# Optimization experiments

Measured on AMD Instinct MI355X. Metric: run time of the kernel, lower is better.

## Reference

```python
import jax, jax.numpy as jnp
import numpy as np

N, E, IN_DIM, OUT_DIM, T = 100000, 1600000, 128, 64, 8
V_THRESHOLD = 1.0
EPS = 1e-7

# ---- Lorentz manifold (curvature -1), time coordinate first ----

def _linner(a, b):
    # Lorentzian inner product <a,b>_L = -a0*b0 + sum_i ai*bi
    return -a[..., 0] * b[..., 0] + jnp.sum(a[..., 1:] * b[..., 1:], axis=-1)

def _proju(z, u):
    # project ambient vector u to tangent space at z (<z,z>_L = -1)
    return u + _linner(z, u)[..., None] * z

def _expmap(z, u):
    un = jnp.sqrt(jnp.maximum(_linner(u, u), EPS))[..., None]
    return jnp.cosh(un) * z + jnp.sinh(un) * u / un

def _dist0(z):
    # geodesic distance to origin o=(1,0,...,0): arccosh(-<o,z>_L) = arccosh(z0)
    return jnp.arccosh(jnp.maximum(z[..., 0], 1.0 + EPS))

# ---- GCNConv (torch_geometric semantics: self-loops + symmetric norm) ----

def _gcn(x, edge_index, W, b):
    src, dst = edge_index[0], edge_index[1]
    loops = jnp.arange(N, dtype=src.dtype)
    src = jnp.concatenate([src, loops])
    dst = jnp.concatenate([dst, loops])
    deg = jax.ops.segment_sum(jnp.ones_like(dst, dtype=x.dtype), dst, num_segments=N)
    dinv = jax.lax.rsqrt(jnp.maximum(deg, 1.0))  # deg >= 1 due to self-loops
    norm = dinv[src] * dinv[dst]                 # [E+N]
    h = x @ W                                    # [N, OUT_DIM]
    out = jax.ops.segment_sum(norm[:, None] * h[src], dst, num_segments=N)
    return out + b


def setup_inputs() -> dict:
    key = jax.random.key(0)
    k1, k2, k3 = jax.random.split(key, 3)
    x = jax.random.normal(k1, (N, IN_DIM), dtype=jnp.float32)
    edge_index = jax.random.randint(k2, (2, E), 0, N, dtype=jnp.int32)
    W = jax.random.normal(k3, (IN_DIM, OUT_DIM), dtype=jnp.float32) / np.sqrt(IN_DIM)
    b = jnp.zeros((OUT_DIM,), dtype=jnp.float32)
    return {"x": x, "edge_index": edge_index, "W": W, "b": b}


def reference(x, edge_index, W, b):
    h = _gcn(x, edge_index, W, b)                       # [N, D]
    origin = jnp.zeros_like(h).at[..., 0].set(1.0)      # manifold origin
    x_seq = jnp.broadcast_to(h, (T,) + h.shape)         # [T, N, D]

    def step(z, x_t):
        u = _proju(z, x_t)                              # input current in T_z M
        z_new = _expmap(z, u)                           # charge along geodesic
        v = _dist0(z_new)                               # membrane potential [N]
        spike = v >= V_THRESHOLD
        z_out = jnp.where(spike[..., None], origin, z_new)  # hard reset
        return z_out, (spike.astype(h.dtype), z_out)

    _, (o_seq, z_seq) = jax.lax.scan(step, origin, x_seq)
    return o_seq, z_seq  # [T, N], [T, N, D]
```

## Files before the change

### kernel.cpp

```cpp
#include <hip/hip_runtime.h>
#include <math.h>

#define IN_DIM_C 128
#define OUT_DIM_C 64
#define T_STEPS 8
#define KC_MAX 512
#define PTILE 2048

__device__ __forceinline__ float4 f4zero() { return make_float4(0.f, 0.f, 0.f, 0.f); }

__global__ __launch_bounds__(256) void k_hist(const int* __restrict__ dst,
                                              int* __restrict__ chist, int E) {
    __shared__ int hh[KC_MAX];
    const int tid = threadIdx.x;
    for (int i = tid; i < KC_MAX; i += 256) hh[i] = 0;
    __syncthreads();
    long base = (long)blockIdx.x * 4096;
    #pragma unroll
    for (int j = 0; j < 16; ++j) {
        long e = base + j * 256 + tid;
        if (e < E) atomicAdd(&hh[dst[e] >> 8], 1);
    }
    __syncthreads();
    for (int i = tid; i < KC_MAX; i += 256)
        if (hh[i]) atomicAdd(&chist[i], hh[i]);
}

__global__ __launch_bounds__(64) void k_scanK(const int* __restrict__ chist,
                                              int* __restrict__ gcursor,
                                              int* __restrict__ offsets,
                                              int kc, int n, int E) {
    int lane = threadIdx.x;
    int carry = 0;
    for (int c = 0; c * 64 < kc; ++c) {
        int idx = c * 64 + lane;
        int v = (idx < kc) ? chist[idx] : 0;
        int x = v;
        #pragma unroll
        for (int off = 1; off < 64; off <<= 1) {
            int t = __shfl_up(x, off, 64);
            if (lane >= off) x += t;
        }
        if (idx < kc) gcursor[idx] = carry + x - v;
        carry += __shfl(x, 63, 64);
    }
    if (lane == 0) offsets[n] = E;
}

__global__ __launch_bounds__(256) void k_gemm(const float* __restrict__ x,
                                              const float* __restrict__ W,
                                              float* __restrict__ h,
                                              int n, int n_groups) {
    __shared__ __align__(16) float Ws[IN_DIM_C * OUT_DIM_C];
    __shared__ __align__(16) float xs[16 * 136];

    for (int i = threadIdx.x; i < IN_DIM_C * OUT_DIM_C / 4; i += 256)
        ((float4*)Ws)[i] = ((const float4*)W)[i];

    const int ln = threadIdx.x >> 4;
    const int dg = threadIdx.x & 15;
    const float4* Ws4 = (const float4*)Ws;

    for (int g = blockIdx.x; g < n_groups; g += gridDim.x) {
        int node_base = g * 16;
        __syncthreads();
        for (int f = threadIdx.x; f < 512; f += 256) {
            int row = f >> 5, c4 = f & 31;
            int node = node_base + row;
            float4 v = f4zero();
            if (node < n) v = *(const float4*)&x[(long)node * IN_DIM_C + c4 * 4];
            *(float4*)&xs[row * 136 + c4 * 4] = v;
        }
        __syncthreads();

        int node = node_base + ln;
        float4 acc = f4zero();
        #pragma unroll
        for (int k = 0; k < IN_DIM_C; k += 4) {
            float4 xv = *(const float4*)&xs[ln * 136 + k];
            float4 w0 = Ws4[(k + 0) * 16 + dg];
            float4 w1 = Ws4[(k + 1) * 16 + dg];
            float4 w2 = Ws4[(k + 2) * 16 + dg];
            float4 w3 = Ws4[(k + 3) * 16 + dg];
            acc.x = fmaf(xv.x, w0.x, acc.x); acc.y = fmaf(xv.x, w0.y, acc.y);
            acc.z = fmaf(xv.x, w0.z, acc.z); acc.w = fmaf(xv.x, w0.w, acc.w);
            acc.x = fmaf(xv.y, w1.x, acc.x); acc.y = fmaf(xv.y, w1.y, acc.y);
            acc.z = fmaf(xv.y, w1.z, acc.z); acc.w = fmaf(xv.y, w1.w, acc.w);
            acc.x = fmaf(xv.z, w2.x, acc.x); acc.y = fmaf(xv.z, w2.y, acc.y);
            acc.z = fmaf(xv.z, w2.z, acc.z); acc.w = fmaf(xv.z, w2.w, acc.w);
            acc.x = fmaf(xv.w, w3.x, acc.x); acc.y = fmaf(xv.w, w3.y, acc.y);
            acc.z = fmaf(xv.w, w3.z, acc.z); acc.w = fmaf(xv.w, w3.w, acc.w);
        }
        if (node < n)
            *(float4*)&h[(long)node * OUT_DIM_C + dg * 4] = acc;
    }
}

__global__ __launch_bounds__(256) void k_part(const int* __restrict__ src,
                                              const int* __restrict__ dst,
                                              int* __restrict__ gcursor,
                                              int* __restrict__ part, int E, int kc) {
    __shared__ int hist[KC_MAX];
    __shared__ int offs[KC_MAX];
    __shared__ int cur[KC_MAX];
    __shared__ int gbase[KC_MAX];
    const int tid = threadIdx.x;
    long base = (long)blockIdx.x * PTILE;

    for (int i = tid; i < KC_MAX; i += 256) hist[i] = 0;
    __syncthreads();
    #pragma unroll
    for (int j = 0; j < PTILE / 256; ++j) {
        long e = base + j * 256 + tid;
        if (e < E) atomicAdd(&hist[dst[e] >> 8], 1);
    }
    __syncthreads();
    if (tid < 64) {
        int carry = 0;
        for (int c = 0; c * 64 < kc; ++c) {
            int idx = c * 64 + tid;
            int v = (idx < kc) ? hist[idx] : 0;
            int x = v;
            #pragma unroll
            for (int off = 1; off < 64; off <<= 1) {
                int t = __shfl_up(x, off, 64);
                if (tid >= off) x += t;
            }
            if (idx < kc) { offs[idx] = carry + x - v; cur[idx] = carry + x - v; }
            carry += __shfl(x, 63, 64);
        }
    }
    __syncthreads();
    for (int b = tid; b < kc; b += 256)
        gbase[b] = hist[b] ? atomicAdd(&gcursor[b], hist[b]) : 0;
    __syncthreads();
    #pragma unroll
    for (int j = 0; j < PTILE / 256; ++j) {
        long e = base + j * 256 + tid;
        if (e < E) {
            int d = dst[e];
            int b = d >> 8;
            int r = atomicAdd(&cur[b], 1);
            part[gbase[b] + r - offs[b]] = (src[e] << 8) | (d & 255);
        }
    }
}

__global__ __launch_bounds__(256) void k_sort(const int* __restrict__ part,
                                              const int* __restrict__ gcursor,
                                              int* __restrict__ part2,
                                              int* __restrict__ offsets,
                                              float* __restrict__ dinv, int n) {
    __shared__ int cnt[256];
    __shared__ int cur[256];
    __shared__ int wsum[4], woff[4];
    const int tid = threadIdx.x;
    const int bkt = blockIdx.x;
    int start = bkt ? gcursor[bkt - 1] : 0;
    int end = gcursor[bkt];

    cnt[tid] = 0;
    __syncthreads();
    for (int i = start + tid; i < end; i += 256)
        atomicAdd(&cnt[part[i] & 255], 1);
    __syncthreads();

    int v = cnt[tid];
    int lane = tid & 63, wv = tid >> 6;
    int x = v;
    #pragma unroll
    for (int off = 1; off < 64; off <<= 1) {
        int t = __shfl_up(x, off, 64);
        if (lane >= off) x += t;
    }
    if (lane == 63) wsum[wv] = x;
    __syncthreads();
    if (tid == 0) { int c = 0; for (int w = 0; w < 4; ++w) { woff[w] = c; c += wsum[w]; } }
    __syncthreads();
    int myloc = woff[wv] + x - v;
    cur[tid] = myloc;
    int node = (bkt << 8) + tid;
    if (node < n) {
        offsets[node] = start + myloc;
        dinv[node] = rsqrtf((float)(v + 1));
    }
    __syncthreads();

    for (int i = start + tid; i < end; i += 256) {
        int p = part[i];
        int r = atomicAdd(&cur[p & 255], 1);
        part2[start + r] = ((unsigned)p) >> 8;
    }
}

__global__ __launch_bounds__(256) void k_pull(const int* __restrict__ offsets,
                                              const int* __restrict__ part2,
                                              const float* __restrict__ dinv,
                                              const float* __restrict__ h,
                                              const float* __restrict__ b,
                                              float* __restrict__ agg, int n) {
    int node = (blockIdx.x * 256 + threadIdx.x) >> 6;
    int lane = threadIdx.x & 63;
    if (node >= n) return;
    int o0 = offsets[node], o1 = offsets[node + 1];
    float dd = dinv[node];
    float acc = fmaf(dd * dd, h[(long)node * OUT_DIM_C + lane], b[lane]);
    int i = o0;
    for (; i + 4 <= o1; i += 4) {
        int s0 = part2[i], s1 = part2[i + 1], s2 = part2[i + 2], s3 = part2[i + 3];
        float n0 = dinv[s0] * dd, n1 = dinv[s1] * dd, n2 = dinv[s2] * dd, n3 = dinv[s3] * dd;
        acc = fmaf(n0, h[(long)s0 * OUT_DIM_C + lane], acc);
        acc = fmaf(n1, h[(long)s1 * OUT_DIM_C + lane], acc);
        acc = fmaf(n2, h[(long)s2 * OUT_DIM_C + lane], acc);
        acc = fmaf(n3, h[(long)s3 * OUT_DIM_C + lane], acc);
    }
    for (; i < o1; ++i) {
        int s = part2[i];
        acc = fmaf(dinv[s] * dd, h[(long)s * OUT_DIM_C + lane], acc);
    }
    agg[(long)node * OUT_DIM_C + lane] = acc;
}

__global__ __launch_bounds__(256) void k_spike(const float* agg,
                                               float* o_seq, float* z_seq, int n) {
    int gid = blockIdx.x * 256 + threadIdx.x;
    int node = gid >> 4;
    int sub = threadIdx.x & 15;
    if (node >= n) return;
    const float s0 = (sub == 0) ? -1.0f : 1.0f;
    int lane0 = (threadIdx.x & 63) & ~15;

    float4 g = *(const float4*)&agg[(long)node * OUT_DIM_C + sub * 4];
    float4 origin = f4zero();
    if (sub == 0) origin.x = 1.0f;

    auto step = [&](float4 z, float4& zn, bool& sp) {
        float p = s0 * z.x * g.x + z.y * g.y + z.z * g.z + z.w * g.w;
        p += __shfl_xor(p, 1, 64);
        p += __shfl_xor(p, 2, 64);
        p += __shfl_xor(p, 4, 64);
        p += __shfl_xor(p, 8, 64);
        float4 u = make_float4(fmaf(p, z.x, g.x), fmaf(p, z.y, g.y),
                               fmaf(p, z.z, g.z), fmaf(p, z.w, g.w));
        float q = s0 * u.x * u.x + u.y * u.y + u.z * u.z + u.w * u.w;
        q += __shfl_xor(q, 1, 64);
        q += __shfl_xor(q, 2, 64);
        q += __shfl_xor(q, 4, 64);
        q += __shfl_xor(q, 8, 64);
        float un = sqrtf(fmaxf(q, 1e-7f));
        float c = coshf(un);
        float sh = sinhf(un) / un;
        zn = make_float4(fmaf(c, z.x, sh * u.x), fmaf(c, z.y, sh * u.y),
                         fmaf(c, z.z, sh * u.z), fmaf(c, z.w, sh * u.w));
        float z0 = __shfl(zn.x, lane0, 64);
        float v = acoshf(fmaxf(z0, 1.0f + 1e-7f));
        sp = (v >= 1.0f);
    };

    float4 z1; bool sp0;
    step(origin, z1, sp0);
    float4 r0 = sp0 ? origin : z1;

    float4 z = origin;
    bool at0 = true;
    for (int t = 0; t < T_STEPS; ++t) {
        float4 zn; bool sp;
        if (at0) { sp = sp0; zn = r0; }
        else {
            step(z, zn, sp);
            if (sp) zn = origin;
        }
        *(float4*)&z_seq[(long)t * n * OUT_DIM_C + (long)node * OUT_DIM_C + sub * 4] = zn;
        if (sub == 0) o_seq[(long)t * n + node] = sp ? 1.0f : 0.0f;
        z = zn;
        at0 = sp;
    }
}

extern "C" void kernel_launch(void* const* d_in, const int* in_sizes, int n_in,
                              void* d_out, int out_size, void* d_ws, size_t ws_size,
                              hipStream_t stream) {
    const float* x  = (const float*)d_in[0];
    const int*   ei = (const int*)d_in[1];
    const float* W  = (const float*)d_in[2];
    const float* b  = (const float*)d_in[3];
    const int N = in_sizes[0] / IN_DIM_C;
    const int E = in_sizes[1] / 2;
    const int KC = (N + 255) >> 8;

    float* out   = (float*)d_out;
    float* o_seq = out;
    float* z_seq = out + (long)T_STEPS * N;

    float* agg     = z_seq;
    float* h       = z_seq + 1L * N * OUT_DIM_C;
    int*   part    = (int*)(z_seq + 2L * N * OUT_DIM_C);
    int*   part2   = (int*)(z_seq + 3L * N * OUT_DIM_C);
    int*   chist   = (int*)(z_seq + 4L * N * OUT_DIM_C);
    int*   gcursor = chist + KC_MAX;
    int*   offsets = gcursor + KC_MAX;
    float* dinv    = (float*)(offsets + N + 1);

    const int* srcp = ei;
    const int* dstp = ei + E;

    hipMemsetAsync(chist, 0, (size_t)KC_MAX * sizeof(int), stream);
    k_hist<<<(E + 4095) / 4096, 256, 0, stream>>>(dstp, chist, E);
    k_scanK<<<1, 64, 0, stream>>>(chist, gcursor, offsets, KC, N, E);

    int n_groups = (N + 15) / 16;
    k_gemm<<<1024, 256, 0, stream>>>(x, W, h, N, n_groups);

    k_part<<<(E + PTILE - 1) / PTILE, 256, 0, stream>>>(srcp, dstp, gcursor, part, E, KC);
    k_sort<<<KC, 256, 0, stream>>>(part, gcursor, part2, offsets, dinv, N);
    k_pull<<<(N * 64 + 255) / 256, 256, 0, stream>>>(offsets, part2, dinv, h, b, agg, N);

    k_spike<<<(N + 15) / 16, 256, 0, stream>>>(agg, o_seq, z_seq, N);
}
```

Before: 434.0 us.

## Register-tile GEMM with 8x8 per-thread outputs and K-chunked shared staging

```diff
diff --git a/kernel.cpp b/kernel.cpp
--- a/kernel.cpp
+++ b/kernel.cpp
@@ -6,6 +6,7 @@
 #define T_STEPS 8
 #define KC_MAX 512
 #define PTILE 2048
+#define GKC 32
 
 __device__ __forceinline__ float4 f4zero() { return make_float4(0.f, 0.f, 0.f, 0.f); }
 
@@ -47,52 +48,78 @@
     if (lane == 0) offsets[n] = E;
 }
 
-__global__ __launch_bounds__(256) void k_gemm(const float* __restrict__ x,
+__global__ __launch_bounds__(128) void k_gemm(const float* __restrict__ x,
                                               const float* __restrict__ W,
-                                              float* __restrict__ h,
-                                              int n, int n_groups) {
-    __shared__ __align__(16) float Ws[IN_DIM_C * OUT_DIM_C];
-    __shared__ __align__(16) float xs[16 * 136];
-
-    for (int i = threadIdx.x; i < IN_DIM_C * OUT_DIM_C / 4; i += 256)
-        ((float4*)Ws)[i] = ((const float4*)W)[i];
-
-    const int ln = threadIdx.x >> 4;
-    const int dg = threadIdx.x & 15;
-    const float4* Ws4 = (const float4*)Ws;
-
-    for (int g = blockIdx.x; g < n_groups; g += gridDim.x) {
-        int node_base = g * 16;
+                                              float* __restrict__ h, int n) {
+    __shared__ __align__(16) float xs[128 * 40];
+    __shared__ __align__(16) float Ws[GKC * OUT_DIM_C];
+
+    const int tid = threadIdx.x;
+    const int cg = tid & 7;
+    const int ng = tid >> 3;
+    const int node_base = blockIdx.x * 128;
+
+    float acc[8][8];
+    #pragma unroll
+    for (int i = 0; i < 8; ++i)
+        #pragma unroll
+        for (int j = 0; j < 8; ++j) acc[i][j] = 0.f;
+
+    for (int c = 0; c < IN_DIM_C / GKC; ++c) {
         __syncthreads();
-        for (int f = threadIdx.x; f < 512; f += 256) {
-            int row = f >> 5, c4 = f & 31;
-            int node = node_base + row;
+        #pragma unroll
+        for (int i = 0; i < 8; ++i) {
+            int idx = tid + i * 128;
+            int nd = idx >> 3, k4 = idx & 7;
+            int node = node_base + nd;
             float4 v = f4zero();
-            if (node < n) v = *(const float4*)&x[(long)node * IN_DIM_C + c4 * 4];
-            *(float4*)&xs[row * 136 + c4 * 4] = v;
+            if (node < n) v = *(const float4*)&x[(long)node * IN_DIM_C + c * GKC + k4 * 4];
+            *(float4*)&xs[nd * 40 + k4 * 4] = v;
+        }
+        #pragma unroll
+        for (int i = 0; i < 4; ++i) {
+            int idx = tid + i * 128;
+            ((float4*)Ws)[idx] = ((const float4*)&W[c * GKC * OUT_DIM_C])[idx];
         }
         __syncthreads();
 
-        int node = node_base + ln;
-        float4 acc = f4zero();
-        #pragma unroll
-        for (int k = 0; k < IN_DIM_C; k += 4) {
-            float4 xv = *(const float4*)&xs[ln * 136 + k];
-            float4 w0 = Ws4[(k + 0) * 16 + dg];
-            float4 w1 = Ws4[(k + 1) * 16 + dg];
-            float4 w2 = Ws4[(k + 2) * 16 + dg];
-            float4 w3 = Ws4[(k + 3) * 16 + dg];
-            acc.x = fmaf(xv.x, w0.x, acc.x); acc.y = fmaf(xv.x, w0.y, acc.y);
-            acc.z = fmaf(xv.x, w0.z, acc.z); acc.w = fmaf(xv.x, w0.w, acc.w);
-            acc.x = fmaf(xv.y, w1.x, acc.x); acc.y = fmaf(xv.y, w1.y, acc.y);
-            acc.z = fmaf(xv.y, w1.z, acc.z); acc.w = fmaf(xv.y, w1.w, acc.w);
-            acc.x = fmaf(xv.z, w2.x, acc.x); acc.y = fmaf(xv.z, w2.y, acc.y);
-            acc.z = fmaf(xv.z, w2.z, acc.z); acc.w = fmaf(xv.z, w2.w, acc.w);
-            acc.x = fmaf(xv.w, w3.x, acc.x); acc.y = fmaf(xv.w, w3.y, acc.y);
-            acc.z = fmaf(xv.w, w3.z, acc.z); acc.w = fmaf(xv.w, w3.w, acc.w);
-        }
-        if (node < n)
-            *(float4*)&h[(long)node * OUT_DIM_C + dg * 4] = acc;
+        #pragma unroll
+        for (int k4 = 0; k4 < GKC / 4; ++k4) {
+            float4 a[8];
+            #pragma unroll
+            for (int i = 0; i < 8; ++i)
+                a[i] = *(const float4*)&xs[(ng * 8 + i) * 40 + k4 * 4];
+            #pragma unroll
+            for (int kk = 0; kk < 4; ++kk) {
+                const float* wr = &Ws[(k4 * 4 + kk) * OUT_DIM_C + cg * 8];
+                float4 b0 = *(const float4*)&wr[0];
+                float4 b1 = *(const float4*)&wr[4];
+                #pragma unroll
+                for (int i = 0; i < 8; ++i) {
+                    float av = (kk == 0) ? a[i].x : (kk == 1) ? a[i].y
+                             : (kk == 2) ? a[i].z : a[i].w;
+                    acc[i][0] = fmaf(av, b0.x, acc[i][0]);
+                    acc[i][1] = fmaf(av, b0.y, acc[i][1]);
+                    acc[i][2] = fmaf(av, b0.z, acc[i][2]);
+                    acc[i][3] = fmaf(av, b0.w, acc[i][3]);
+                    acc[i][4] = fmaf(av, b1.x, acc[i][4]);
+                    acc[i][5] = fmaf(av, b1.y, acc[i][5]);
+                    acc[i][6] = fmaf(av, b1.z, acc[i][6]);
+                    acc[i][7] = fmaf(av, b1.w, acc[i][7]);
+                }
+            }
+        }
+    }
+
+    #pragma unroll
+    for (int i = 0; i < 8; ++i) {
+        int node = node_base + ng * 8 + i;
+        if (node < n) {
+            *(float4*)&h[(long)node * OUT_DIM_C + cg * 8] =
+                make_float4(acc[i][0], acc[i][1], acc[i][2], acc[i][3]);
+            *(float4*)&h[(long)node * OUT_DIM_C + cg * 8 + 4] =
+                make_float4(acc[i][4], acc[i][5], acc[i][6], acc[i][7]);
+        }
     }
 }
 
@@ -308,8 +335,7 @@
     k_hist<<<(E + 4095) / 4096, 256, 0, stream>>>(dstp, chist, E);
     k_scanK<<<1, 64, 0, stream>>>(chist, gcursor, offsets, KC, N, E);
 
-    int n_groups = (N + 15) / 16;
-    k_gemm<<<1024, 256, 0, stream>>>(x, W, h, N, n_groups);
+    k_gemm<<<(N + 127) / 128, 128, 0, stream>>>(x, W, h, N);
 
     k_part<<<(E + PTILE - 1) / PTILE, 256, 0, stream>>>(srcp, dstp, gcursor, part, E, KC);
     k_sort<<<KC, 256, 0, stream>>>(part, gcursor, part2, offsets, dinv, N);
```

After: 455.4 us. +4.9%, slower.
